# Performance work log

Measured on AMD Instinct MI355X. Metric: run time of the kernel, lower is better.

Reference implementation:

```python
import jax, jax.numpy as jnp
import numpy as np

H = 8      # num_attention_heads
DH = 96    # attention_head_size
LN_EPS = 1e-5


def setup_inputs() -> dict:
    key = jax.random.key(0)
    ks = jax.random.split(key, 12)
    B, S, D = 2, 768, 768
    sc = 0.02
    return {
        "hidden_states": jax.random.normal(ks[0], (B, S, D), jnp.float32),
        "distance_matrix": jax.random.uniform(ks[1], (B, S, S), jnp.float32) * 20.0,
        "angle_matrix": jax.random.uniform(ks[2], (B, S, S), jnp.float32) * np.pi,
        "attention_mask": jnp.ones((B, S), jnp.float32),
        "Wq": jax.random.normal(ks[3], (D, D), jnp.float32) * sc,
        "bq": jnp.zeros((D,), jnp.float32),
        "Wk": jax.random.normal(ks[4], (D, D), jnp.float32) * sc,
        "bk": jnp.zeros((D,), jnp.float32),
        "Wv": jax.random.normal(ks[5], (D, D), jnp.float32) * sc,
        "bv": jnp.zeros((D,), jnp.float32),
        "Wd": jax.random.normal(ks[6], (DH,), jnp.float32) * sc,
        "bd": jnp.zeros((DH,), jnp.float32),
        "Wa": jax.random.normal(ks[7], (DH,), jnp.float32) * sc,
        "ba": jnp.zeros((DH,), jnp.float32),
        "Wo": jax.random.normal(ks[8], (D, D), jnp.float32) * sc,
        "bo": jnp.zeros((D,), jnp.float32),
        "ln_g": jnp.ones((D,), jnp.float32),
        "ln_b": jnp.zeros((D,), jnp.float32),
    }


def _heads(x, B, S):
    # [B,S,D] -> [B,H,S,DH]
    return x.reshape(B, S, H, DH).transpose(0, 2, 1, 3)


def reference(hidden_states, distance_matrix, angle_matrix, attention_mask,
              Wq, bq, Wk, bk, Wv, bv, Wd, bd, Wa, ba, Wo, bo, ln_g, ln_b):
    B, S, D = hidden_states.shape
    q = _heads(hidden_states @ Wq.T + bq, B, S)   # [B,H,S,DH]
    k = _heads(hidden_states @ Wk.T + bk, B, S)
    v = _heads(hidden_states @ Wv.T + bv, B, S)

    scores = jnp.einsum('bhid,bhjd->bhij', q, k) / jnp.sqrt(jnp.float32(DH))

    # distance / angle relative-position biases: emb[b,i,j,:] = dist[b,i,j]*Wd + bd
    dist_emb = distance_matrix[..., None] * Wd + bd   # [B,S,S,DH]
    scores = scores + jnp.einsum('bhid,bijd->bhij', q, dist_emb)
    ang_emb = angle_matrix[..., None] * Wa + ba       # [B,S,S,DH]
    scores = scores + jnp.einsum('bhid,bijd->bhij', q, ang_emb)

    # key mask, broadcast over heads and query positions
    scores = scores + (1.0 - attention_mask)[:, None, None, :] * -10000.0

    probs = jax.nn.softmax(scores, axis=-1)           # [B,H,S,S]
    ctx = jnp.einsum('bhij,bhjd->bhid', probs, v)
    ctx = ctx.transpose(0, 2, 1, 3).reshape(B, S, D)  # [B,S,D]

    out = ctx @ Wo.T + bo
    x = out + hidden_states
    mu = jnp.mean(x, axis=-1, keepdims=True)
    var = jnp.var(x, axis=-1, keepdims=True)
    out = (x - mu) * jax.lax.rsqrt(var + LN_EPS) * ln_g + ln_b
    return out, probs
```

## Files before the change

kernel.cpp:

```cpp
#include <hip/hip_runtime.h>
#include <stdint.h>

#define B_  2
#define S_  768
#define D_  768
#define H_  8
#define DH_ 96

typedef unsigned short ushort_t;
typedef __bf16 bf16x8 __attribute__((ext_vector_type(8)));
typedef float  f32x4  __attribute__((ext_vector_type(4)));
typedef _Float16 f16x4 __attribute__((ext_vector_type(4)));

__device__ inline ushort_t f2bf(float f) {
    union { float f; unsigned int u; } v; v.f = f;
    unsigned int u = v.u;
    unsigned int r = u + 0x7fffu + ((u >> 16) & 1u);
    return (ushort_t)(r >> 16);
}
__device__ inline float bf2f(ushort_t u) {
    union { unsigned int i; float f; } c; c.i = ((unsigned int)u) << 16;
    return c.f;
}
__device__ inline ushort_t f2h(float f) {
    union { _Float16 h; ushort_t u; } c; c.h = (_Float16)f; return c.u;
}

__device__ inline void glds16(const void* gp, void* lp) {
    auto g = reinterpret_cast<const __attribute__((address_space(1))) uint32_t*>(
        reinterpret_cast<uintptr_t>(gp));
    auto l = reinterpret_cast<__attribute__((address_space(3))) uint32_t*>(
        reinterpret_cast<uintptr_t>(lp));
    __builtin_amdgcn_global_load_lds(g, l, 16, 0, 0);
}

#define SBAR()  { __builtin_amdgcn_sched_barrier(0); __builtin_amdgcn_s_barrier(); \
                  __builtin_amdgcn_sched_barrier(0); }
#define WAIT_VM(N) { asm volatile("s_waitcnt vmcnt(" #N ")" ::: "memory"); \
                     __builtin_amdgcn_sched_barrier(0); }

__global__ __launch_bounds__(256) void k_convert(
        const float* __restrict__ X, const float* __restrict__ Wq,
        const float* __restrict__ Wk, const float* __restrict__ Wv,
        const float* __restrict__ Wo, const float* __restrict__ distm,
        const float* __restrict__ angm,
        ushort_t* __restrict__ Xb, ushort_t* __restrict__ Wb,
        ushort_t* __restrict__ Dh, ushort_t* __restrict__ Ah) {
    __shared__ float tlds[64][65];
    const int NX4 = (B_ * S_ * D_) / 4;
    const int NW4 = (D_ * D_) / 4;
    const int bid = blockIdx.x, tid = threadIdx.x;
    if (bid < 3456) {
        int i = bid * 256 + tid;
        float4 v;
        ushort_t* dst;
        if (i < NX4) {
            v = ((const float4*)X)[i];
            dst = Xb + i * 4;
        } else {
            int wi = i - NX4;
            int sel = wi / NW4;
            int off = wi - sel * NW4;
            const float* src = (sel == 0) ? Wq : (sel == 1) ? Wk : (sel == 2) ? Wv : Wo;
            v = ((const float4*)src)[off];
            dst = Wb + wi * 4;
        }
        ushort4 o;
        o.x = f2bf(v.x); o.y = f2bf(v.y); o.z = f2bf(v.z); o.w = f2bf(v.w);
        *(ushort4*)dst = o;
        return;
    }
    int tidx = bid - 3456;
    int mat = tidx / 288, t2 = tidx - mat * 288;
    int b = t2 / 144, t3 = t2 - b * 144;
    int rt = t3 / 12, ct = t3 - rt * 12;
    const float* src = (mat ? angm : distm) + ((size_t)(b * S_ + rt * 64)) * S_ + ct * 64;
    ushort_t* dstm = mat ? Ah : Dh;
    {
        int tr = tid >> 4, tc4 = tid & 15;
        #pragma unroll
        for (int k = 0; k < 4; ++k) {
            int row = tr + k * 16;
            float4 v4 = *(const float4*)(src + (size_t)row * S_ + tc4 * 4);
            tlds[row][tc4 * 4 + 0] = v4.x;
            tlds[row][tc4 * 4 + 1] = v4.y;
            tlds[row][tc4 * 4 + 2] = v4.z;
            tlds[row][tc4 * 4 + 3] = v4.w;
        }
    }
    __syncthreads();
    {
        int row = tid & 63, s4b = tid >> 6;
        #pragma unroll
        for (int k = 0; k < 4; ++k) {
            int s4l = s4b * 4 + k;
            ushort4 o4;
            o4.x = f2h(tlds[row][s4l * 4 + 0]);
            o4.y = f2h(tlds[row][s4l * 4 + 1]);
            o4.z = f2h(tlds[row][s4l * 4 + 2]);
            o4.w = f2h(tlds[row][s4l * 4 + 3]);
            *(ushort4*)&dstm[(((size_t)b * 192 + ct * 16 + s4l) * 768 + rt * 64 + row) * 4] = o4;
        }
    }
}

__device__ inline void gemm64_tbuf(
        const ushort_t* __restrict__ A, int lda,
        const ushort_t* __restrict__ Bt, int ldb,
        int K, int m0, int n0,
        ushort_t* As, ushort_t* Bs, f32x4 acc[2][2]) {
    const int tid  = threadIdx.x;
    const int lane = tid & 63, wave = tid >> 6;
    const int wm = (wave >> 1) * 32, wn = (wave & 1) * 32;
    const int fr = lane & 15, fk = (lane >> 4) * 8;
    const ushort_t* Ap = A  + (size_t)(m0 + wave * 16 + (lane >> 2)) * lda + (lane & 3) * 8;
    const ushort_t* Bp = Bt + (size_t)(n0 + wave * 16 + (lane >> 2)) * ldb + (lane & 3) * 8;
    glds16(Ap,      As + wave * 512);
    glds16(Bp,      Bs + wave * 512);
    glds16(Ap + 32, As + 2048 + wave * 512);
    glds16(Bp + 32, Bs + 2048 + wave * 512);
    for (int kt = 0; kt < K; kt += 32) {
        const int cur = (kt >> 5) % 3;
        if (kt + 32 < K) { WAIT_VM(2) } else { WAIT_VM(0) }
        SBAR()
        if (kt + 64 < K) {
            const int nb = ((kt >> 5) + 2) % 3;
            glds16(Ap + kt + 64, As + nb * 2048 + wave * 512);
            glds16(Bp + kt + 64, Bs + nb * 2048 + wave * 512);
        }
        const ushort_t* Ab = As + cur * 2048;
        const ushort_t* Bb = Bs + cur * 2048;
        bf16x8 a0 = *(const bf16x8*)&Ab[(wm      + fr) * 32 + fk];
        bf16x8 a1 = *(const bf16x8*)&Ab[(wm + 16 + fr) * 32 + fk];
        bf16x8 b0 = *(const bf16x8*)&Bb[(wn      + fr) * 32 + fk];
        bf16x8 b1 = *(const bf16x8*)&Bb[(wn + 16 + fr) * 32 + fk];
        acc[0][0] = __builtin_amdgcn_mfma_f32_16x16x32_bf16(a0, b0, acc[0][0], 0, 0, 0);
        acc[0][1] = __builtin_amdgcn_mfma_f32_16x16x32_bf16(a0, b1, acc[0][1], 0, 0, 0);
        acc[1][0] = __builtin_amdgcn_mfma_f32_16x16x32_bf16(a1, b0, acc[1][0], 0, 0, 0);
        acc[1][1] = __builtin_amdgcn_mfma_f32_16x16x32_bf16(a1, b1, acc[1][1], 0, 0, 0);
    }
}

__global__ __launch_bounds__(256) void k_qkv(
        const ushort_t* __restrict__ Xb, const ushort_t* __restrict__ Wb,
        const float* __restrict__ bq, const float* __restrict__ bk,
        const float* __restrict__ bv,
        ushort_t* __restrict__ Qb, ushort_t* __restrict__ Kb,
        ushort_t* __restrict__ Vtb) {
    __shared__ __align__(16) ushort_t As[3 * 64 * 32];
    __shared__ __align__(16) ushort_t Bs[3 * 64 * 32];
    f32x4 acc[2][2];
    #pragma unroll
    for (int i = 0; i < 2; i++)
        #pragma unroll
        for (int j = 0; j < 2; j++) acc[i][j] = (f32x4){0.f, 0.f, 0.f, 0.f};
    const int m0 = blockIdx.y * 64, n0 = blockIdx.x * 64;
    gemm64_tbuf(Xb, D_, Wb, D_, D_, m0, n0, As, Bs, acc);
    const int lane = threadIdx.x & 63, wave = threadIdx.x >> 6;
    const int wm = (wave >> 1) * 32, wn = (wave & 1) * 32;
    #pragma unroll
    for (int ni = 0; ni < 2; ni++) {
        int gcol = n0 + wn + ni * 16 + (lane & 15);
        int gsel = gcol / D_, d768 = gcol - gsel * D_;
        int h = d768 / DH_, d = d768 - h * DH_;
        float bias = (gsel == 0 ? bq : (gsel == 1 ? bk : bv))[d768];
        #pragma unroll
        for (int mi = 0; mi < 2; mi++) {
            int grow0 = m0 + wm + mi * 16 + (lane >> 4) * 4;
            int b = grow0 / S_, s0 = grow0 - b * S_;
            int bh = b * H_ + h;
            if (gsel == 2) {
                ushort4 o4;
                o4.x = f2bf(acc[mi][ni][0] + bias);
                o4.y = f2bf(acc[mi][ni][1] + bias);
                o4.z = f2bf(acc[mi][ni][2] + bias);
                o4.w = f2bf(acc[mi][ni][3] + bias);
                int p = s0 >> 7, wv = (s0 >> 4) & 3, gq = (s0 >> 2) & 3;
                int e0 = (s0 >> 6) & 1;
                size_t off = ((size_t)bh * 73728) + p * 12288 + wv * 3072
                           + (d >> 4) * 512 + (gq * 16 + (d & 15)) * 8 + e0 * 4;
                *(ushort4*)&Vtb[off] = o4;
            } else if (gsel == 1) {
                #pragma unroll
                for (int r = 0; r < 4; r++)
                    Kb[(((size_t)bh * 12 + (d >> 3)) * S_ + s0 + r) * 8 + (d & 7)] =
                        f2bf(acc[mi][ni][r] + bias);
            } else {
                #pragma unroll
                for (int r = 0; r < 4; r++)
                    Qb[((size_t)bh * S_ + s0 + r) * DH_ + d] = f2bf(acc[mi][ni][r] + bias);
            }
        }
    }
}

__global__ __launch_bounds__(256, 3) void k_flash(
        const ushort_t* __restrict__ Qb, const ushort_t* __restrict__ Kb,
        const ushort_t* __restrict__ Vtb,
        const float* __restrict__ Wd, const float* __restrict__ bd,
        const float* __restrict__ Wa, const float* __restrict__ ba,
        const ushort_t* __restrict__ Dh, const ushort_t* __restrict__ Ah,
        const float* __restrict__ mask,
        float* __restrict__ probs, ushort_t* __restrict__ Ctxb) {
    __shared__ float mstat[64];
    __shared__ float lstat[64];
    __shared__ float ctxred[1600];
    const int idx = blockIdx.x;
    const int bh = idx & 15, t = idx >> 4;
    const int b = bh >> 3, h = bh & 7;
    const int r0 = t * 16;
    const int tid = threadIdx.x, lane = tid & 63, w = tid >> 6;
    const int frn = lane & 15, g = lane >> 4;
    const ushort_t* Qbh = Qb + (size_t)bh * S_ * DH_;
    const ushort_t* Kbh = Kb + (size_t)bh * 12 * S_ * 8;

    #pragma unroll
    for (int i = 0; i < 7; ++i) {
        int z = tid + i * 256;
        if (z < 1600) ctxred[z] = 0.f;
    }

    bf16x8 aq0, aq1, aq2;
    {
        const ushort_t* qp = Qbh + (size_t)(r0 + frn) * DH_ + g * 8;
        aq0 = *(const bf16x8*)qp;
        aq1 = *(const bf16x8*)(qp + 32);
        aq2 = *(const bf16x8*)(qp + 64);
    }
    float qc0 = 0.f, qc1 = 0.f, qc2 = 0.f;
    #pragma unroll
    for (int f = 0; f < 3; ++f) {
        bf16x8 aq = (f == 0) ? aq0 : (f == 1) ? aq1 : aq2;
        #pragma unroll
        for (int e = 0; e < 8; ++e) {
            int d = f * 32 + g * 8 + e;
            float qv = (float)aq[e];
            qc0 += qv * Wd[d];
            qc1 += qv * Wa[d];
            qc2 += qv * (bd[d] + ba[d]);
        }
    }
    qc0 += __shfl_xor(qc0, 16); qc0 += __shfl_xor(qc0, 32);
    qc1 += __shfl_xor(qc1, 16); qc1 += __shfl_xor(qc1, 32);
    qc2 += __shfl_xor(qc2, 16); qc2 += __shfl_xor(qc2, 32);

    const float isq = 0.10206207261596577f;

    f32x4 acc[12];
    const ushort_t* kbase = Kbh + ((size_t)g * S_ + 16 * w + frn) * 8;
    const ushort_t* dbase = Dh + ((size_t)(b * 192 + w * 4 + g) * 768 + r0 + frn) * 4;
    const ushort_t* abase = Ah + ((size_t)(b * 192 + w * 4 + g) * 768 + r0 + frn) * 4;
    const float*    mbase = mask + b * S_ + w * 16 + g * 4;
    struct Ch { bf16x8 k0, k1, k2; uint2 dd, aa; float4 m4; };
    auto LDC = [&](int c) {
        Ch r;
        const ushort_t* kp = kbase + (size_t)c * 64 * 8;
        r.k0 = *(const bf16x8*)kp;
        r.k1 = *(const bf16x8*)(kp + (size_t)4 * S_ * 8);
        r.k2 = *(const bf16x8*)(kp + (size_t)8 * S_ * 8);
        r.dd = *(const uint2*)(dbase + (size_t)c * 16 * 768 * 4);
        r.aa = *(const uint2*)(abase + (size_t)c * 16 * 768 * 4);
        r.m4 = *(const float4*)(mbase + c * 64);
        return r;
    };
    Ch p0 = LDC(0), p1 = LDC(1);
    #pragma unroll
    for (int c = 0; c < 12; ++c) {
        Ch nx;
        if (c < 10) nx = LDC(c + 2); else nx = p1;
        f32x4 ca = (f32x4){0.f, 0.f, 0.f, 0.f};
        ca = __builtin_amdgcn_mfma_f32_16x16x32_bf16(p0.k0, aq0, ca, 0, 0, 0);
        ca = __builtin_amdgcn_mfma_f32_16x16x32_bf16(p0.k1, aq1, ca, 0, 0, 0);
        ca = __builtin_amdgcn_mfma_f32_16x16x32_bf16(p0.k2, aq2, ca, 0, 0, 0);
        union { uint2 u; f16x4 hh; } dd, aa;
        dd.u = p0.dd; aa.u = p0.aa;
        f32x4 o;
        o[0] = ca[0] * isq + (float)dd.hh[0] * qc0 + (float)aa.hh[0] * qc1 + qc2 + (1.f - p0.m4.x) * -10000.f;
        o[1] = ca[1] * isq + (float)dd.hh[1] * qc0 + (float)aa.hh[1] * qc1 + qc2 + (1.f - p0.m4.y) * -10000.f;
        o[2] = ca[2] * isq + (float)dd.hh[2] * qc0 + (float)aa.hh[2] * qc1 + qc2 + (1.f - p0.m4.z) * -10000.f;
        o[3] = ca[3] * isq + (float)dd.hh[3] * qc0 + (float)aa.hh[3] * qc1 + qc2 + (1.f - p0.m4.w) * -10000.f;
        acc[c] = o;
        p0 = p1; p1 = nx;
    }

    float mx = -1e30f;
    #pragma unroll
    for (int c = 0; c < 12; ++c)
        #pragma unroll
        for (int r = 0; r < 4; ++r) mx = fmaxf(mx, acc[c][r]);
    mx = fmaxf(mx, __shfl_xor(mx, 16));
    mx = fmaxf(mx, __shfl_xor(mx, 32));
    if (g == 0) mstat[w * 16 + frn] = mx;
    __syncthreads();
    float mf = fmaxf(fmaxf(mstat[frn], mstat[16 + frn]),
                     fmaxf(mstat[32 + frn], mstat[48 + frn]));
    float sum = 0.f;
    #pragma unroll
    for (int c = 0; c < 12; ++c)
        #pragma unroll
        for (int r = 0; r < 4; ++r) {
            float e = __expf(acc[c][r] - mf);
            acc[c][r] = e;
            sum += e;
        }
    sum += __shfl_xor(sum, 16);
    sum += __shfl_xor(sum, 32);
    if (g == 0) lstat[w * 16 + frn] = sum;
    __syncthreads();
    float inv = 1.f / (lstat[frn] + lstat[16 + frn] + lstat[32 + frn] + lstat[48 + frn]);

    f32x4 accO[6];
    #pragma unroll
    for (int i = 0; i < 6; ++i) accO[i] = (f32x4){0.f, 0.f, 0.f, 0.f};
    float* prow = probs + ((size_t)bh * S_ + r0 + frn) * S_ + w * 16 + g * 4;
    const ushort_t* vfb = Vtb + (size_t)bh * 73728 + w * 3072 + lane * 8;
    bf16x8 vcur[6];
    #pragma unroll
    for (int nt = 0; nt < 6; ++nt)
        vcur[nt] = *(const bf16x8*)(vfb + nt * 512);
    #pragma unroll
    for (int p = 0; p < 6; ++p) {
        const int c = 2 * p;
        bf16x8 vnx[6];
        #pragma unroll
        for (int nt = 0; nt < 6; ++nt)
            vnx[nt] = (p < 5) ? *(const bf16x8*)(vfb + (p + 1) * 12288 + nt * 512)
                              : vcur[nt];
        f32x4 pw;
        pw[0] = acc[c][0] * inv; pw[1] = acc[c][1] * inv;
        pw[2] = acc[c][2] * inv; pw[3] = acc[c][3] * inv;
        __builtin_nontemporal_store(pw, (f32x4*)(prow + c * 64));
        pw[0] = acc[c + 1][0] * inv; pw[1] = acc[c + 1][1] * inv;
        pw[2] = acc[c + 1][2] * inv; pw[3] = acc[c + 1][3] * inv;
        __builtin_nontemporal_store(pw, (f32x4*)(prow + (c + 1) * 64));
        union { bf16x8 v; ushort_t u[8]; } pa;
        #pragma unroll
        for (int r = 0; r < 4; ++r) {
            pa.u[r]     = f2bf(acc[c][r]);
            pa.u[r + 4] = f2bf(acc[c + 1][r]);
        }
        #pragma unroll
        for (int nt = 0; nt < 6; ++nt)
            accO[nt] = __builtin_amdgcn_mfma_f32_16x16x32_bf16(pa.v, vcur[nt], accO[nt], 0, 0, 0);
        #pragma unroll
        for (int nt = 0; nt < 6; ++nt) vcur[nt] = vnx[nt];
    }

    #pragma unroll
    for (int nt = 0; nt < 6; ++nt)
        #pragma unroll
        for (int r = 0; r < 4; ++r)
            atomicAdd(&ctxred[(4 * g + r) * 100 + nt * 16 + frn], accO[nt][r]);
    __syncthreads();
    {
        int zr = tid >> 4, zc = tid & 15;
        float ivr = 1.f / (lstat[zr] + lstat[16 + zr] + lstat[32 + zr] + lstat[48 + zr]);
        ushort_t* crow = Ctxb + ((size_t)b * S_ + r0 + zr) * D_ + h * DH_;
        #pragma unroll
        for (int i = 0; i < 6; ++i)
            crow[i * 16 + zc] = f2bf(ctxred[zr * 100 + i * 16 + zc] * ivr);
    }
}

__global__ __launch_bounds__(256) void k_out(
        const ushort_t* __restrict__ Ctxb, const ushort_t* __restrict__ Wob,
        const float* __restrict__ bo, const float* __restrict__ hidden,
        float* __restrict__ xbuf) {
    __shared__ __align__(16) ushort_t As[3 * 64 * 32];
    __shared__ __align__(16) ushort_t Bs[3 * 64 * 32];
    f32x4 acc[2][2];
    #pragma unroll
    for (int i = 0; i < 2; i++)
        #pragma unroll
        for (int j = 0; j < 2; j++) acc[i][j] = (f32x4){0.f, 0.f, 0.f, 0.f};
    const int m0 = blockIdx.y * 64, n0 = blockIdx.x * 64;
    gemm64_tbuf(Ctxb, D_, Wob, D_, D_, m0, n0, As, Bs, acc);
    const int lane = threadIdx.x & 63, wave = threadIdx.x >> 6;
    const int wm = (wave >> 1) * 32, wn = (wave & 1) * 32;
    #pragma unroll
    for (int ni = 0; ni < 2; ni++) {
        int gcol = n0 + wn + ni * 16 + (lane & 15);
        float bias = bo[gcol];
        #pragma unroll
        for (int mi = 0; mi < 2; mi++) {
            #pragma unroll
            for (int r = 0; r < 4; r++) {
                int grow = m0 + wm + mi * 16 + (lane >> 4) * 4 + r;
                xbuf[(size_t)grow * D_ + gcol] =
                    acc[mi][ni][r] + bias + hidden[(size_t)grow * D_ + gcol];
            }
        }
    }
}

__global__ __launch_bounds__(256) void k_ln(
        const float* __restrict__ xbuf, const float* __restrict__ g,
        const float* __restrict__ bb, float* __restrict__ out) {
    const float* x = xbuf + (size_t)blockIdx.x * D_;
    const int t = threadIdx.x;
    float a0 = x[t], a1 = x[t + 256], a2 = x[t + 512];
    float s = a0 + a1 + a2;
    float ss = a0 * a0 + a1 * a1 + a2 * a2;
    __shared__ float r1[4], r2[4];
    #pragma unroll
    for (int o = 32; o > 0; o >>= 1) { s += __shfl_down(s, o); ss += __shfl_down(ss, o); }
    if ((t & 63) == 0) { r1[t >> 6] = s; r2[t >> 6] = ss; }
    __syncthreads();
    float ts = r1[0] + r1[1] + r1[2] + r1[3];
    float tss = r2[0] + r2[1] + r2[2] + r2[3];
    float mu = ts * (1.0f / D_);
    float var = tss * (1.0f / D_) - mu * mu;
    float rstd = rsqrtf(var + 1e-5f);
    float* o = out + (size_t)blockIdx.x * D_;
    o[t]       = (a0 - mu) * rstd * g[t]       + bb[t];
    o[t + 256] = (a1 - mu) * rstd * g[t + 256] + bb[t + 256];
    o[t + 512] = (a2 - mu) * rstd * g[t + 512] + bb[t + 512];
}

extern "C" void kernel_launch(void* const* d_in, const int* in_sizes, int n_in,
                              void* d_out, int out_size, void* d_ws, size_t ws_size,
                              hipStream_t stream) {
    const float* X     = (const float*)d_in[0];
    const float* distm = (const float*)d_in[1];
    const float* angm  = (const float*)d_in[2];
    const float* mask  = (const float*)d_in[3];
    const float* Wq    = (const float*)d_in[4];
    const float* bq    = (const float*)d_in[5];
    const float* Wk    = (const float*)d_in[6];
    const float* bk    = (const float*)d_in[7];
    const float* Wv    = (const float*)d_in[8];
    const float* bv    = (const float*)d_in[9];
    const float* Wd    = (const float*)d_in[10];
    const float* bd    = (const float*)d_in[11];
    const float* Wa    = (const float*)d_in[12];
    const float* ba    = (const float*)d_in[13];
    const float* Wo    = (const float*)d_in[14];
    const float* bo    = (const float*)d_in[15];
    const float* ln_g  = (const float*)d_in[16];
    const float* ln_b  = (const float*)d_in[17];

    float* outp  = (float*)d_out;
    float* probs = (float*)d_out + (size_t)B_ * S_ * D_;

    char* ws = (char*)d_ws;
    ushort_t* Xb    = (ushort_t*)(ws + 0);
    ushort_t* Wb    = (ushort_t*)(ws + 2359296);
    ushort_t* Qb    = (ushort_t*)(ws + 7077888);
    ushort_t* Kb    = (ushort_t*)(ws + 9437184);
    ushort_t* Vtb   = (ushort_t*)(ws + 11796480);
    ushort_t* Ctxb  = (ushort_t*)(ws + 14155776);
    float*    xbuf  = (float*)   (ws + 16662528);
    ushort_t* Dh    = (ushort_t*)(ws + 16662528);
    ushort_t* Ah    = (ushort_t*)(ws + 16662528 + 2359296);

    k_convert<<<4032, 256, 0, stream>>>(X, Wq, Wk, Wv, Wo, distm, angm, Xb, Wb, Dh, Ah);
    k_qkv<<<dim3(36, 24), 256, 0, stream>>>(Xb, Wb, bq, bk, bv, Qb, Kb, Vtb);
    k_flash<<<768, 256, 0, stream>>>(Qb, Kb, Vtb, Wd, bd, Wa, ba, Dh, Ah, mask, probs, Ctxb);
    k_out<<<dim3(12, 24), 256, 0, stream>>>(Ctxb, Wb + (size_t)2304 * 768, bo, X, xbuf);
    k_ln<<<1536, 256, 0, stream>>>(xbuf, ln_g, ln_b, outp);
}
```

Before: 179.3 us.

## Enlarge QKV GEMM tiles and fold distance/angle transposes into the QKV launch

Moves the distance/angle fp32-to-fp16 transpose blocks out of the convert kernel and into a combined QKV kernel, so those memory-bound blocks run alongside the GEMM blocks in the same grid. The QKV GEMM switches from 64x64 tiles with 256 threads to 128x128 tiles with 512 threads, giving each wave a 4x2 MFMA fragment for more register-level reuse and fewer blocks (216 GEMM plus 576 transpose blocks). The larger tile uses 48KB LDS and more accumulators, which may lower occupancy. The 216 GEMM blocks may also leave CUs underfilled.

```diff
diff --git a/kernel.cpp b/kernel.cpp
--- a/kernel.cpp
+++ b/kernel.cpp
@@ -42,64 +42,150 @@
 __global__ __launch_bounds__(256) void k_convert(
         const float* __restrict__ X, const float* __restrict__ Wq,
         const float* __restrict__ Wk, const float* __restrict__ Wv,
-        const float* __restrict__ Wo, const float* __restrict__ distm,
-        const float* __restrict__ angm,
-        ushort_t* __restrict__ Xb, ushort_t* __restrict__ Wb,
-        ushort_t* __restrict__ Dh, ushort_t* __restrict__ Ah) {
-    __shared__ float tlds[64][65];
+        const float* __restrict__ Wo,
+        ushort_t* __restrict__ Xb, ushort_t* __restrict__ Wb) {
     const int NX4 = (B_ * S_ * D_) / 4;
     const int NW4 = (D_ * D_) / 4;
+    int i = blockIdx.x * 256 + threadIdx.x;
+    float4 v;
+    ushort_t* dst;
+    if (i < NX4) {
+        v = ((const float4*)X)[i];
+        dst = Xb + i * 4;
+    } else {
+        int wi = i - NX4;
+        int sel = wi / NW4;
+        int off = wi - sel * NW4;
+        const float* src = (sel == 0) ? Wq : (sel == 1) ? Wk : (sel == 2) ? Wv : Wo;
+        v = ((const float4*)src)[off];
+        dst = Wb + wi * 4;
+    }
+    ushort4 o;
+    o.x = f2bf(v.x); o.y = f2bf(v.y); o.z = f2bf(v.z); o.w = f2bf(v.w);
+    *(ushort4*)dst = o;
+}
+
+__global__ __launch_bounds__(512) void k_qkvt(
+        const ushort_t* __restrict__ Xb, const ushort_t* __restrict__ Wb,
+        const float* __restrict__ bq, const float* __restrict__ bk,
+        const float* __restrict__ bv,
+        const float* __restrict__ distm, const float* __restrict__ angm,
+        ushort_t* __restrict__ Qb, ushort_t* __restrict__ Kb,
+        ushort_t* __restrict__ Vtb,
+        ushort_t* __restrict__ Dh, ushort_t* __restrict__ Ah) {
+    __shared__ __align__(16) char sm[49152];
     const int bid = blockIdx.x, tid = threadIdx.x;
-    if (bid < 3456) {
-        int i = bid * 256 + tid;
-        float4 v;
-        ushort_t* dst;
-        if (i < NX4) {
-            v = ((const float4*)X)[i];
-            dst = Xb + i * 4;
-        } else {
-            int wi = i - NX4;
-            int sel = wi / NW4;
-            int off = wi - sel * NW4;
-            const float* src = (sel == 0) ? Wq : (sel == 1) ? Wk : (sel == 2) ? Wv : Wo;
-            v = ((const float4*)src)[off];
-            dst = Wb + wi * 4;
-        }
-        ushort4 o;
-        o.x = f2bf(v.x); o.y = f2bf(v.y); o.z = f2bf(v.z); o.w = f2bf(v.w);
-        *(ushort4*)dst = o;
+    if (bid >= 216) {
+        float* tlds = (float*)sm;
+        int tidx = bid - 216;
+        int mat = tidx / 288, t2 = tidx - mat * 288;
+        int b = t2 / 144, t3 = t2 - b * 144;
+        int rt = t3 / 12, ct = t3 - rt * 12;
+        const float* src = (mat ? angm : distm) + ((size_t)(b * S_ + rt * 64)) * S_ + ct * 64;
+        ushort_t* dstm = mat ? Ah : Dh;
+        {
+            int tr = tid >> 4, tc4 = tid & 15;
+            #pragma unroll
+            for (int k = 0; k < 2; ++k) {
+                int row = tr + k * 32;
+                float4 v4 = *(const float4*)(src + (size_t)row * S_ + tc4 * 4);
+                tlds[row * 65 + tc4 * 4 + 0] = v4.x;
+                tlds[row * 65 + tc4 * 4 + 1] = v4.y;
+                tlds[row * 65 + tc4 * 4 + 2] = v4.z;
+                tlds[row * 65 + tc4 * 4 + 3] = v4.w;
+            }
+        }
+        __syncthreads();
+        {
+            int row = tid & 63, s4b = tid >> 6;
+            #pragma unroll
+            for (int k = 0; k < 2; ++k) {
+                int s4l = s4b * 2 + k;
+                ushort4 o4;
+                o4.x = f2h(tlds[row * 65 + s4l * 4 + 0]);
+                o4.y = f2h(tlds[row * 65 + s4l * 4 + 1]);
+                o4.z = f2h(tlds[row * 65 + s4l * 4 + 2]);
+                o4.w = f2h(tlds[row * 65 + s4l * 4 + 3]);
+                *(ushort4*)&dstm[(((size_t)b * 192 + ct * 16 + s4l) * 768 + rt * 64 + row) * 4] = o4;
+            }
+        }
         return;
     }
-    int tidx = bid - 3456;
-    int mat = tidx / 288, t2 = tidx - mat * 288;
-    int b = t2 / 144, t3 = t2 - b * 144;
-    int rt = t3 / 12, ct = t3 - rt * 12;
-    const float* src = (mat ? angm : distm) + ((size_t)(b * S_ + rt * 64)) * S_ + ct * 64;
-    ushort_t* dstm = mat ? Ah : Dh;
-    {
-        int tr = tid >> 4, tc4 = tid & 15;
-        #pragma unroll
-        for (int k = 0; k < 4; ++k) {
-            int row = tr + k * 16;
-            float4 v4 = *(const float4*)(src + (size_t)row * S_ + tc4 * 4);
-            tlds[row][tc4 * 4 + 0] = v4.x;
-            tlds[row][tc4 * 4 + 1] = v4.y;
-            tlds[row][tc4 * 4 + 2] = v4.z;
-            tlds[row][tc4 * 4 + 3] = v4.w;
-        }
-    }
-    __syncthreads();
-    {
-        int row = tid & 63, s4b = tid >> 6;
-        #pragma unroll
-        for (int k = 0; k < 4; ++k) {
-            int s4l = s4b * 4 + k;
-            ushort4 o4;
-            o4.x = f2h(tlds[row][s4l * 4 + 0]);
-            o4.y = f2h(tlds[row][s4l * 4 + 1]);
-            o4.z = f2h(tlds[row][s4l * 4 + 2]);
-            o4.w = f2h(tlds[row][s4l * 4 + 3]);
-            *(ushort4*)&dstm[(((size_t)b * 192 + ct * 16 + s4l) * 768 + rt * 64 + row) * 4] = o4;
+    ushort_t* As = (ushort_t*)sm;
+    ushort_t* Bs = (ushort_t*)(sm + 24576);
+    const int by = bid / 18, bx = bid - by * 18;
+    const int m0 = by * 128, n0 = bx * 128;
+    const int lane = tid & 63, w = tid >> 6;
+    const int wr = w >> 2, wc = w & 3;
+    const int wm = wr * 64, wn = wc * 32;
+    const int frn = lane & 15, fko = (lane >> 4) * 8, frg4 = (lane >> 4) * 4;
+    const ushort_t* Ap = Xb + (size_t)(m0 + w * 16 + (lane >> 2)) * D_ + (lane & 3) * 8;
+    const ushort_t* Bp = Wb + (size_t)(n0 + w * 16 + (lane >> 2)) * D_ + (lane & 3) * 8;
+    f32x4 acc[4][2];
+    #pragma unroll
+    for (int i = 0; i < 4; ++i)
+        #pragma unroll
+        for (int j = 0; j < 2; ++j) acc[i][j] = (f32x4){0.f, 0.f, 0.f, 0.f};
+    glds16(Ap,      As + w * 512);
+    glds16(Bp,      Bs + w * 512);
+    glds16(Ap + 32, As + 4096 + w * 512);
+    glds16(Bp + 32, Bs + 4096 + w * 512);
+    for (int kt = 0; kt < D_; kt += 32) {
+        const int cur = (kt >> 5) % 3;
+        if (kt + 32 < D_) { WAIT_VM(2) } else { WAIT_VM(0) }
+        SBAR()
+        if (kt + 64 < D_) {
+            const int nb = ((kt >> 5) + 2) % 3;
+            glds16(Ap + kt + 64, As + nb * 4096 + w * 512);
+            glds16(Bp + kt + 64, Bs + nb * 4096 + w * 512);
+        }
+        const ushort_t* Ab = As + cur * 4096;
+        const ushort_t* Bb = Bs + cur * 4096;
+        bf16x8 af[4], bfr[2];
+        #pragma unroll
+        for (int i = 0; i < 4; ++i)
+            af[i] = *(const bf16x8*)&Ab[(wm + i * 16 + frn) * 32 + fko];
+        #pragma unroll
+        for (int j = 0; j < 2; ++j)
+            bfr[j] = *(const bf16x8*)&Bb[(wn + j * 16 + frn) * 32 + fko];
+        #pragma unroll
+        for (int i = 0; i < 4; ++i)
+            #pragma unroll
+            for (int j = 0; j < 2; ++j)
+                acc[i][j] = __builtin_amdgcn_mfma_f32_16x16x32_bf16(af[i], bfr[j], acc[i][j], 0, 0, 0);
+    }
+    #pragma unroll
+    for (int j = 0; j < 2; ++j) {
+        int gcol = n0 + wn + j * 16 + frn;
+        int gsel = gcol / D_, d768 = gcol - gsel * D_;
+        int h = d768 / DH_, d = d768 - h * DH_;
+        float bias = (gsel == 0 ? bq : (gsel == 1 ? bk : bv))[d768];
+        #pragma unroll
+        for (int i = 0; i < 4; ++i) {
+            int grow0 = m0 + wm + i * 16 + frg4;
+            int b = grow0 / S_, s0 = grow0 - b * S_;
+            int bh = b * H_ + h;
+            if (gsel == 2) {
+                ushort4 o4;
+                o4.x = f2bf(acc[i][j][0] + bias);
+                o4.y = f2bf(acc[i][j][1] + bias);
+                o4.z = f2bf(acc[i][j][2] + bias);
+                o4.w = f2bf(acc[i][j][3] + bias);
+                int p = s0 >> 7, wv = (s0 >> 4) & 3, gq = (s0 >> 2) & 3;
+                int e0 = (s0 >> 6) & 1;
+                size_t off = ((size_t)bh * 73728) + p * 12288 + wv * 3072
+                           + (d >> 4) * 512 + (gq * 16 + (d & 15)) * 8 + e0 * 4;
+                *(ushort4*)&Vtb[off] = o4;
+            } else if (gsel == 1) {
+                #pragma unroll
+                for (int r = 0; r < 4; r++)
+                    Kb[(((size_t)bh * 12 + (d >> 3)) * S_ + s0 + r) * 8 + (d & 7)] =
+                        f2bf(acc[i][j][r] + bias);
+            } else {
+                #pragma unroll
+                for (int r = 0; r < 4; r++)
+                    Qb[((size_t)bh * S_ + s0 + r) * DH_ + d] = f2bf(acc[i][j][r] + bias);
+            }
         }
     }
 }
@@ -141,59 +227,6 @@
     }
 }
 
-__global__ __launch_bounds__(256) void k_qkv(
-        const ushort_t* __restrict__ Xb, const ushort_t* __restrict__ Wb,
-        const float* __restrict__ bq, const float* __restrict__ bk,
-        const float* __restrict__ bv,
-        ushort_t* __restrict__ Qb, ushort_t* __restrict__ Kb,
-        ushort_t* __restrict__ Vtb) {
-    __shared__ __align__(16) ushort_t As[3 * 64 * 32];
-    __shared__ __align__(16) ushort_t Bs[3 * 64 * 32];
-    f32x4 acc[2][2];
-    #pragma unroll
-    for (int i = 0; i < 2; i++)
-        #pragma unroll
-        for (int j = 0; j < 2; j++) acc[i][j] = (f32x4){0.f, 0.f, 0.f, 0.f};
-    const int m0 = blockIdx.y * 64, n0 = blockIdx.x * 64;
-    gemm64_tbuf(Xb, D_, Wb, D_, D_, m0, n0, As, Bs, acc);
-    const int lane = threadIdx.x & 63, wave = threadIdx.x >> 6;
-    const int wm = (wave >> 1) * 32, wn = (wave & 1) * 32;
-    #pragma unroll
-    for (int ni = 0; ni < 2; ni++) {
-        int gcol = n0 + wn + ni * 16 + (lane & 15);
-        int gsel = gcol / D_, d768 = gcol - gsel * D_;
-        int h = d768 / DH_, d = d768 - h * DH_;
-        float bias = (gsel == 0 ? bq : (gsel == 1 ? bk : bv))[d768];
-        #pragma unroll
-        for (int mi = 0; mi < 2; mi++) {
-            int grow0 = m0 + wm + mi * 16 + (lane >> 4) * 4;
-            int b = grow0 / S_, s0 = grow0 - b * S_;
-            int bh = b * H_ + h;
-            if (gsel == 2) {
-                ushort4 o4;
-                o4.x = f2bf(acc[mi][ni][0] + bias);
-                o4.y = f2bf(acc[mi][ni][1] + bias);
-                o4.z = f2bf(acc[mi][ni][2] + bias);
-                o4.w = f2bf(acc[mi][ni][3] + bias);
-                int p = s0 >> 7, wv = (s0 >> 4) & 3, gq = (s0 >> 2) & 3;
-                int e0 = (s0 >> 6) & 1;
-                size_t off = ((size_t)bh * 73728) + p * 12288 + wv * 3072
-                           + (d >> 4) * 512 + (gq * 16 + (d & 15)) * 8 + e0 * 4;
-                *(ushort4*)&Vtb[off] = o4;
-            } else if (gsel == 1) {
-                #pragma unroll
-                for (int r = 0; r < 4; r++)
-                    Kb[(((size_t)bh * 12 + (d >> 3)) * S_ + s0 + r) * 8 + (d & 7)] =
-                        f2bf(acc[mi][ni][r] + bias);
-            } else {
-                #pragma unroll
-                for (int r = 0; r < 4; r++)
-                    Qb[((size_t)bh * S_ + s0 + r) * DH_ + d] = f2bf(acc[mi][ni][r] + bias);
-            }
-        }
-    }
-}
-
 __global__ __launch_bounds__(256, 3) void k_flash(
         const ushort_t* __restrict__ Qb, const ushort_t* __restrict__ Kb,
         const ushort_t* __restrict__ Vtb,
@@ -453,8 +486,8 @@
     ushort_t* Dh    = (ushort_t*)(ws + 16662528);
     ushort_t* Ah    = (ushort_t*)(ws + 16662528 + 2359296);
 
-    k_convert<<<4032, 256, 0, stream>>>(X, Wq, Wk, Wv, Wo, distm, angm, Xb, Wb, Dh, Ah);
-    k_qkv<<<dim3(36, 24), 256, 0, stream>>>(Xb, Wb, bq, bk, bv, Qb, Kb, Vtb);
+    k_convert<<<3456, 256, 0, stream>>>(X, Wq, Wk, Wv, Wo, Xb, Wb);
+    k_qkvt<<<792, 512, 0, stream>>>(Xb, Wb, bq, bk, bv, distm, angm, Qb, Kb, Vtb, Dh, Ah);
     k_flash<<<768, 256, 0, stream>>>(Qb, Kb, Vtb, Wd, bd, Wa, ba, Dh, Ah, mask, probs, Ctxb);
     k_out<<<dim3(12, 24), 256, 0, stream>>>(Ctxb, Wb + (size_t)2304 * 768, bo, X, xbuf);
     k_ln<<<1536, 256, 0, stream>>>(xbuf, ln_g, ln_b, outp);
```

Measured after the change: 174.7 us. 1.03x faster.
